# Optimization experiments

Hardware: AMD Instinct MI355X
Metric: run time of the kernel (lower is better)

## Reference

```python
import jax, jax.numpy as jnp
import numpy as np

C = 512  # in_channels

def _maxpool2x2(t):
    # t: [B, c, H, W] -> [B, c, H//2, W//2]
    B, c, H, W = t.shape
    return t.reshape(B, c, H // 2, 2, W // 2, 2).max(axis=(3, 5))

def setup_inputs() -> dict:
    key = jax.random.key(0)
    ks = jax.random.split(key, 6)
    B, H, W = 16, 64, 64
    x = jax.random.normal(ks[0], (B, C, H, W), dtype=jnp.float32)
    # 1x1 conv weights (spectral norm is just a static rescale of the weight;
    # we model the post-normalized weight directly). Shapes: [out_c, in_c].
    scale = 0.02
    w_theta = jax.random.normal(ks[1], (C // 8, C), dtype=jnp.float32) * scale
    w_phi = jax.random.normal(ks[2], (C // 8, C), dtype=jnp.float32) * scale
    w_g = jax.random.normal(ks[3], (C // 2, C), dtype=jnp.float32) * scale
    w_o = jax.random.normal(ks[4], (C, C // 2), dtype=jnp.float32) * scale
    gamma = jnp.asarray(0.5, dtype=jnp.float32)  # nonzero so attention path matters
    return {"x": x, "w_theta": w_theta, "w_phi": w_phi, "w_g": w_g,
            "w_o": w_o, "gamma": gamma}

def reference(x, w_theta, w_phi, w_g, w_o, gamma):
    B, c, H, W = x.shape
    N = H * W
    M = N // 4
    # 1x1 convs == channel matmuls
    theta = jnp.einsum('oc,bchw->bohw', w_theta, x)            # [B, C/8, H, W]
    phi = _maxpool2x2(jnp.einsum('oc,bchw->bohw', w_phi, x))   # [B, C/8, H/2, W/2]
    g = _maxpool2x2(jnp.einsum('oc,bchw->bohw', w_g, x))       # [B, C/2, H/2, W/2]
    theta = theta.reshape(B, c // 8, N)
    phi = phi.reshape(B, c // 8, M)
    g = g.reshape(B, c // 2, M)
    # attention: softmax over keys (last dim)
    scores = jnp.einsum('bdn,bdm->bnm', theta, phi)            # [B, N, M]
    beta = jax.nn.softmax(scores, axis=-1)
    o = jnp.einsum('bvm,bnm->bvn', g, beta)                    # [B, C/2, N]
    o = o.reshape(B, c // 2, H, W)
    o = jnp.einsum('ov,bvhw->bohw', w_o, o)                    # [B, C, H, W]
    return gamma * o + x
```

## Files before the change

kernel.cpp:

```cpp
#include <hip/hip_runtime.h>
#include <hip/hip_fp16.h>

typedef unsigned int u32;
typedef unsigned short u16;
typedef u32 __attribute__((may_alias)) u32a;
typedef u16 __attribute__((may_alias)) u16a;
typedef uint4 __attribute__((may_alias)) uint4a;
typedef uint2 __attribute__((may_alias)) uint2a;
typedef float __attribute__((may_alias)) f32a;
typedef float4 __attribute__((may_alias)) float4a;

typedef __attribute__((ext_vector_type(8))) short short8v;
typedef __attribute__((ext_vector_type(4))) float float4v;

union Frag { uint4 q; short8v s; u16 u[8]; };
union F4 { float4 v; float f[4]; };

#define BATCH 16
#define CIN   512
#define NPIX  4096
#define DD    64
#define VV    256
#define MM    1024

__device__ __forceinline__ float b2f(u16 u) {
  union { u32 i; float f; } v; v.i = ((u32)u) << 16; return v.f;
}
__device__ __forceinline__ u16 f2b(float f) {
  union { float f; u32 i; } v; v.f = f;
  u32 u = v.i;
  u32 r = (u + 0x7fffu + ((u >> 16) & 1u)) >> 16;
  return (u16)r;
}
__device__ __forceinline__ u16 f2h(float f) { return __half_as_ushort(__float2half(f)); }
__device__ __forceinline__ float h2f(u16 u) { return __half2float(__ushort_as_half(u)); }

__device__ __forceinline__ u32 cvtpk(float lo, float hi) {
  u32 r;
  asm("v_cvt_pk_bf16_f32 %0, %1, %2" : "=v"(r) : "v"(lo), "v"(hi));
  return r;
}

__device__ __forceinline__ float dot2(u32 a, u32 b, float c) {
  union { u32 i; float f; } a0, a1, b0, b1;
  a0.i = a << 16; a1.i = a & 0xffff0000u;
  b0.i = b << 16; b1.i = b & 0xffff0000u;
  return fmaf(a1.f, b1.f, fmaf(a0.f, b0.f, c));
}

__global__ __launch_bounds__(256) void k_detect(const void* __restrict__ x,
                                                u32* __restrict__ meta) {
  __shared__ int bad[256];
  const int t = threadIdx.x;
  float f = b2f(((const u16a*)x)[2 * t]);
  float a = fabsf(f);
  bad[t] = (a >= 1e-6f && a <= 100.f) ? 0 : 1;
  __syncthreads();
  if (t == 0) {
    int s = 0;
#pragma unroll 16
    for (int i = 0; i < 256; ++i) s += bad[i];
    meta[0] = (s > 64) ? 1u : 0u;
  }
}

__global__ __launch_bounds__(256) void k_cvt(
    const void* __restrict__ wt, const void* __restrict__ wp,
    const void* __restrict__ wg, const void* __restrict__ wo,
    const void* __restrict__ gm, const u32* __restrict__ meta,
    u16* __restrict__ wbf, float* __restrict__ gout) {
  const int flag = (int)meta[0];
  const int i = blockIdx.x * 256 + threadIdx.x;
  const void* src; int j;
  if (i < 32768)       { src = wt; j = i; }
  else if (i < 65536)  { src = wp; j = i - 32768; }
  else if (i < 196608) { src = wg; j = i - 65536; }
  else                 { src = wo; j = i - 196608; }
  wbf[i] = flag ? f2b(((const f32a*)src)[j]) : ((const u16a*)src)[j];
  if (i == 0)
    gout[0] = flag ? ((const f32a*)gm)[0] : b2f(((const u16a*)gm)[0]);
}

__global__ __launch_bounds__(256) void k_proj(
    const void* __restrict__ x, const u16* __restrict__ w_all,
    const u32* __restrict__ meta,
    u16* __restrict__ theta, u16* __restrict__ phi_t, u16* __restrict__ g)
{
  __shared__ __align__(16) u16 xs[128][136];
  const int tid  = threadIdx.x;
  const int lane = tid & 63;
  const int wv   = tid >> 6;
  const int lg   = lane >> 4;
  const int lr   = lane & 15;
  const int blk  = blockIdx.x;
  const int b    = blk >> 5;
  const int pxt  = blk & 31;
  const int n0   = pxt * 128;
  const int rbase = wv * 96;
  const int flag = (int)meta[0];

  float4v acc[6][8];
#pragma unroll
  for (int i = 0; i < 6; ++i)
#pragma unroll
    for (int j = 0; j < 8; ++j) acc[i][j] = (float4v){0.f, 0.f, 0.f, 0.f};

  const int pg = tid & 15;
  const int cg = tid >> 4;

  for (int cc = 0; cc < 4; ++cc) {
    const int c0 = cc * 128;
    __syncthreads();
    if (flag) {
      const f32a* src = (const f32a*)x +
          ((size_t)(b * CIN + c0 + cg * 8)) * NPIX + n0 + pg * 4;
#pragma unroll
      for (int cq = 0; cq < 2; ++cq) {
        const f32a* s4 = src + (size_t)(cq * 4) * NPIX;
        F4 a0, a1, a2, a3, b0, b1, b2, b3;
        a0.v = *(const float4a*)(s4);
        b0.v = *(const float4a*)(s4 + 64);
        a1.v = *(const float4a*)(s4 + NPIX);
        b1.v = *(const float4a*)(s4 + NPIX + 64);
        a2.v = *(const float4a*)(s4 + 2 * (size_t)NPIX);
        b2.v = *(const float4a*)(s4 + 2 * (size_t)NPIX + 64);
        a3.v = *(const float4a*)(s4 + 3 * (size_t)NPIX);
        b3.v = *(const float4a*)(s4 + 3 * (size_t)NPIX + 64);
        const int colb = cg * 8 + cq * 4;
#pragma unroll
        for (int j = 0; j < 4; ++j) {
          uint2 wd; wd.x = cvtpk(a0.f[j], a1.f[j]); wd.y = cvtpk(a2.f[j], a3.f[j]);
          *(uint2a*)&xs[pg * 4 + j][colb] = wd;
          uint2 vd; vd.x = cvtpk(b0.f[j], b1.f[j]); vd.y = cvtpk(b2.f[j], b3.f[j]);
          *(uint2a*)&xs[64 + pg * 4 + j][colb] = vd;
        }
      }
    } else {
#pragma unroll 8
      for (int it = 0; it < 64; ++it) {
        int idx = tid + it * 256;
        int cl = idx >> 7, px = idx & 127;
        xs[px][cl] = ((const u16a*)x)[((size_t)(b * CIN + c0 + cl)) * NPIX + (n0 + px)];
      }
    }
    __syncthreads();

#pragma unroll
    for (int kk = 0; kk < 4; ++kk) {
      short8v bfr[8];
#pragma unroll
      for (int pt = 0; pt < 8; ++pt) {
        Frag f; f.q = *(const uint4a*)&xs[pt * 16 + lr][kk * 32 + lg * 8];
        bfr[pt] = f.s;
      }
#pragma unroll
      for (int rt = 0; rt < 6; ++rt) {
        Frag af;
        af.q = *(const uint4a*)(w_all +
            (size_t)(rbase + rt * 16 + lr) * CIN + c0 + kk * 32 + lg * 8);
#pragma unroll
        for (int pt = 0; pt < 8; ++pt)
          acc[rt][pt] = __builtin_amdgcn_mfma_f32_16x16x32_bf16(af.s, bfr[pt], acc[rt][pt], 0, 0, 0);
      }
    }
  }

#pragma unroll
  for (int rt = 0; rt < 6; ++rt) {
    const int rowb = rbase + rt * 16;
    if (rowb < 64) {
#pragma unroll
      for (int pt = 0; pt < 8; ++pt)
#pragma unroll
        for (int r = 0; r < 4; ++r) {
          int row = rowb + lg * 4 + r;
          theta[((size_t)(b * DD + row)) * NPIX + n0 + pt * 16 + lr] = f2b(acc[rt][pt][r]);
        }
    } else {
#pragma unroll
      for (int pt = 0; pt < 4; ++pt)
#pragma unroll
        for (int r = 0; r < 4; ++r) {
          int row = rowb + lg * 4 + r;
          float pm = fmaxf(acc[rt][pt][r], acc[rt][pt + 4][r]);
          float po = fmaxf(pm, __shfl_xor(pm, 1));
          if (!(lr & 1)) {
            int m = pxt * 32 + pt * 8 + (lr >> 1);
            if (row < 128) phi_t[((size_t)(b * MM + m)) * DD + (row - 64)] = f2b(po);
            else           g[((size_t)(b * VV + (row - 128))) * MM + m]    = f2b(po);
          }
        }
    }
  }
}

__global__ __launch_bounds__(512, 4) void k_attn2(
    const u16* __restrict__ theta, const u16* __restrict__ phi_t,
    const u16* __restrict__ g, u16* __restrict__ o_t)
{
  __shared__ __align__(16) u32 sc[32 * 516];
  __shared__ float pmax8[32][8];
  __shared__ float psum[32][16];
  __shared__ float sinv_s[32];

  const int tid  = threadIdx.x;
  const int lane = tid & 63;
  const int wv   = tid >> 6;
  const int lg   = lane >> 4;
  const int lr   = lane & 15;
  const int bid  = blockIdx.x;
  const int swz  = ((bid & 7) << 8) | (bid >> 3);
  const int b    = swz >> 7;
  const int bqt  = swz & 127;
  const int nq0  = bqt * 32;

  u16a* sc16 = (u16a*)sc;

  short8v qa[2][2];
#pragma unroll
  for (int qt = 0; qt < 2; ++qt)
#pragma unroll
    for (int kk = 0; kk < 2; ++kk) {
      Frag f;
#pragma unroll
      for (int i = 0; i < 8; ++i) {
        int d = kk * 32 + lg * 8 + i;
        f.u[i] = theta[((size_t)(b * DD + d)) * NPIX + nq0 + qt * 16 + lr];
      }
      qa[qt][kk] = f.s;
    }

  {
    float mx0 = -3.0e38f, mx1 = -3.0e38f;
    const u16* ptw = phi_t + ((size_t)(b * MM) + wv * 128 + lr) * DD + lg * 8;
    uint4 f0 = *(const uint4a*)(ptw);
    uint4 f1 = *(const uint4a*)(ptw + 32);
#pragma unroll
    for (int mt = 0; mt < 8; ++mt) {
      const int mtn = (mt < 7) ? mt + 1 : 7;
      uint4 n0v = *(const uint4a*)(ptw + (size_t)mtn * 16 * DD);
      uint4 n1v = *(const uint4a*)(ptw + (size_t)mtn * 16 * DD + 32);
      Frag a0; a0.q = f0; Frag a1; a1.q = f1;
      float4v s0 = {0.f, 0.f, 0.f, 0.f}, s1 = {0.f, 0.f, 0.f, 0.f};
      s0 = __builtin_amdgcn_mfma_f32_16x16x32_bf16(a0.s, qa[0][0], s0, 0, 0, 0);
      s0 = __builtin_amdgcn_mfma_f32_16x16x32_bf16(a1.s, qa[0][1], s0, 0, 0, 0);
      s1 = __builtin_amdgcn_mfma_f32_16x16x32_bf16(a0.s, qa[1][0], s1, 0, 0, 0);
      s1 = __builtin_amdgcn_mfma_f32_16x16x32_bf16(a1.s, qa[1][1], s1, 0, 0, 0);
      float c0 = fminf(fmaxf(s0[0], -6.0e4f), 6.0e4f);
      float c1 = fminf(fmaxf(s0[1], -6.0e4f), 6.0e4f);
      float c2 = fminf(fmaxf(s0[2], -6.0e4f), 6.0e4f);
      float c3 = fminf(fmaxf(s0[3], -6.0e4f), 6.0e4f);
      mx0 = fmaxf(mx0, fmaxf(fmaxf(c0, c1), fmaxf(c2, c3)));
      uint2 w0;
      w0.x = (u32)f2h(c0) | ((u32)f2h(c1) << 16);
      w0.y = (u32)f2h(c2) | ((u32)f2h(c3) << 16);
      *(uint2a*)&sc16[(size_t)lr * 1032 + wv * 128 + mt * 16 + lg * 4] = w0;
      float d0 = fminf(fmaxf(s1[0], -6.0e4f), 6.0e4f);
      float d1 = fminf(fmaxf(s1[1], -6.0e4f), 6.0e4f);
      float d2 = fminf(fmaxf(s1[2], -6.0e4f), 6.0e4f);
      float d3 = fminf(fmaxf(s1[3], -6.0e4f), 6.0e4f);
      mx1 = fmaxf(mx1, fmaxf(fmaxf(d0, d1), fmaxf(d2, d3)));
      uint2 w1;
      w1.x = (u32)f2h(d0) | ((u32)f2h(d1) << 16);
      w1.y = (u32)f2h(d2) | ((u32)f2h(d3) << 16);
      *(uint2a*)&sc16[(size_t)(16 + lr) * 1032 + wv * 128 + mt * 16 + lg * 4] = w1;
      f0 = n0v; f1 = n1v;
    }
    mx0 = fmaxf(mx0, __shfl_xor(mx0, 16));
    mx0 = fmaxf(mx0, __shfl_xor(mx0, 32));
    mx1 = fmaxf(mx1, __shfl_xor(mx1, 16));
    mx1 = fmaxf(mx1, __shfl_xor(mx1, 32));
    if (lane < 16) {
      pmax8[lr][wv]      = mx0;
      pmax8[16 + lr][wv] = mx1;
    }
  }
  __syncthreads();

  const int q  = tid & 31;
  const int sg = tid >> 5;
  {
    float maxq = pmax8[q][0];
#pragma unroll
    for (int i = 1; i < 8; ++i) maxq = fmaxf(maxq, pmax8[q][i]);
    float ssum = 0.f;
#pragma unroll 4
    for (int kp = 0; kp < 32; ++kp) {
      int kk = (kp + sg) & 31;
      int idx = q * 516 + sg * 32 + kk;
      u32 raw = sc[idx];
      float f0 = h2f((u16)(raw & 0xffffu));
      float f1 = h2f((u16)(raw >> 16));
      float e0 = __expf(fminf(f0 - maxq, 0.f));
      float e1 = __expf(fminf(f1 - maxq, 0.f));
      ssum += e0 + e1;
      sc[idx] = (u32)f2b(e0) | ((u32)f2b(e1) << 16);
    }
    psum[q][sg] = ssum;
    __syncthreads();
    float tot = 0.f;
#pragma unroll
    for (int i = 0; i < 16; ++i) tot += psum[q][i];
    if (sg == 0) sinv_s[q] = 1.f / tot;
  }
  __syncthreads();

  {
    const u16* gv0 = g + (size_t)b * (VV * MM) + ((size_t)(wv * 32) + lr) * MM + lg * 8;
    const u16* gv1 = gv0 + (size_t)16 * MM;
    const u16* p0b = sc16 + (size_t)lr * 1032 + lg * 8;
    const u16* p1b = p0b + (size_t)16 * 1032;

    float4v a00 = {0.f,0.f,0.f,0.f}, a01 = {0.f,0.f,0.f,0.f};
    float4v a10 = {0.f,0.f,0.f,0.f}, a11 = {0.f,0.f,0.f,0.f};

    uint4 ga0 = *(const uint4a*)(gv0);
    uint4 ga1 = *(const uint4a*)(gv1);
    uint4 pa0 = *(const uint4a*)(p0b);
    uint4 pa1 = *(const uint4a*)(p1b);
    uint4 gb0 = *(const uint4a*)(gv0 + 32);
    uint4 gb1 = *(const uint4a*)(gv1 + 32);
    uint4 pb0 = *(const uint4a*)(p0b + 32);
    uint4 pb1 = *(const uint4a*)(p1b + 32);

#pragma unroll 4
    for (int ms = 0; ms < 32; ms += 2) {
      const int m2 = (ms + 2 < 32) ? ms + 2 : 30;
      const int m3 = (ms + 3 < 32) ? ms + 3 : 31;
      uint4 gc0 = *(const uint4a*)(gv0 + m2 * 32);
      uint4 gc1 = *(const uint4a*)(gv1 + m2 * 32);
      uint4 pc0 = *(const uint4a*)(p0b + m2 * 32);
      uint4 pc1 = *(const uint4a*)(p1b + m2 * 32);
      {
        Frag x0, x1, y0, y1; x0.q = ga0; x1.q = ga1; y0.q = pa0; y1.q = pa1;
        a00 = __builtin_amdgcn_mfma_f32_16x16x32_bf16(x0.s, y0.s, a00, 0, 0, 0);
        a01 = __builtin_amdgcn_mfma_f32_16x16x32_bf16(x0.s, y1.s, a01, 0, 0, 0);
        a10 = __builtin_amdgcn_mfma_f32_16x16x32_bf16(x1.s, y0.s, a10, 0, 0, 0);
        a11 = __builtin_amdgcn_mfma_f32_16x16x32_bf16(x1.s, y1.s, a11, 0, 0, 0);
      }
      uint4 gd0 = *(const uint4a*)(gv0 + m3 * 32);
      uint4 gd1 = *(const uint4a*)(gv1 + m3 * 32);
      uint4 pd0 = *(const uint4a*)(p0b + m3 * 32);
      uint4 pd1 = *(const uint4a*)(p1b + m3 * 32);
      {
        Frag x0, x1, y0, y1; x0.q = gb0; x1.q = gb1; y0.q = pb0; y1.q = pb1;
        a00 = __builtin_amdgcn_mfma_f32_16x16x32_bf16(x0.s, y0.s, a00, 0, 0, 0);
        a01 = __builtin_amdgcn_mfma_f32_16x16x32_bf16(x0.s, y1.s, a01, 0, 0, 0);
        a10 = __builtin_amdgcn_mfma_f32_16x16x32_bf16(x1.s, y0.s, a10, 0, 0, 0);
        a11 = __builtin_amdgcn_mfma_f32_16x16x32_bf16(x1.s, y1.s, a11, 0, 0, 0);
      }
      ga0 = gc0; ga1 = gc1; pa0 = pc0; pa1 = pc1;
      gb0 = gd0; gb1 = gd1; pb0 = pd0; pb1 = pd1;
    }

    const float si0 = sinv_s[lr];
    const float si1 = sinv_s[16 + lr];
    {
      uint2 wd;
      wd.x = cvtpk(a00[0] * si0, a00[1] * si0);
      wd.y = cvtpk(a00[2] * si0, a00[3] * si0);
      *(uint2a*)(o_t + ((size_t)(b * NPIX + nq0 + lr)) * VV + wv * 32 + lg * 4) = wd;
      wd.x = cvtpk(a01[0] * si1, a01[1] * si1);
      wd.y = cvtpk(a01[2] * si1, a01[3] * si1);
      *(uint2a*)(o_t + ((size_t)(b * NPIX + nq0 + 16 + lr)) * VV + wv * 32 + lg * 4) = wd;
      wd.x = cvtpk(a10[0] * si0, a10[1] * si0);
      wd.y = cvtpk(a10[2] * si0, a10[3] * si0);
      *(uint2a*)(o_t + ((size_t)(b * NPIX + nq0 + lr)) * VV + wv * 32 + 16 + lg * 4) = wd;
      wd.x = cvtpk(a11[0] * si1, a11[1] * si1);
      wd.y = cvtpk(a11[2] * si1, a11[3] * si1);
      *(uint2a*)(o_t + ((size_t)(b * NPIX + nq0 + 16 + lr)) * VV + wv * 32 + 16 + lg * 4) = wd;
    }
  }
}

__global__ __launch_bounds__(256, 4) void k_oproj(
    const u16* __restrict__ o_t, const u16* __restrict__ wo,
    const void* __restrict__ x, const float* __restrict__ gamma_p,
    const u32* __restrict__ meta, void* __restrict__ out)
{
  const int tid  = threadIdx.x;
  const int lane = tid & 63;
  const int wv   = tid >> 6;
  const int lg   = lane >> 4;
  const int lr   = lane & 15;
  const int bid  = blockIdx.x;
  const int swz  = ((bid & 7) << 9) | (bid >> 3);
  const int b    = swz >> 8;
  const int nt   = (swz >> 1) & 127;
  const int och  = swz & 1;
  const int n0   = nt * 32;
  const int ocb  = och * 256 + wv * 64;
  const int flag = (int)meta[0];

  float4v acc[4][2];
#pragma unroll
  for (int j = 0; j < 4; ++j)
#pragma unroll
    for (int t = 0; t < 2; ++t) acc[j][t] = (float4v){0.f, 0.f, 0.f, 0.f};

  const u16* obl = o_t + ((size_t)(b * NPIX) + n0 + lr) * VV;
  const u16* wbl = wo + (size_t)(ocb + lr) * VV;

#pragma unroll 2
  for (int kk = 0; kk < 8; ++kk) {
    const int ko = kk * 32 + lg * 8;
    Frag a0, a1, w0, w1, w2, w3;
    a0.q = *(const uint4a*)(obl + ko);
    a1.q = *(const uint4a*)(obl + (size_t)16 * VV + ko);
    w0.q = *(const uint4a*)(wbl + ko);
    w1.q = *(const uint4a*)(wbl + (size_t)16 * VV + ko);
    w2.q = *(const uint4a*)(wbl + (size_t)32 * VV + ko);
    w3.q = *(const uint4a*)(wbl + (size_t)48 * VV + ko);
    acc[0][0] = __builtin_amdgcn_mfma_f32_16x16x32_bf16(a0.s, w0.s, acc[0][0], 0, 0, 0);
    acc[0][1] = __builtin_amdgcn_mfma_f32_16x16x32_bf16(a1.s, w0.s, acc[0][1], 0, 0, 0);
    acc[1][0] = __builtin_amdgcn_mfma_f32_16x16x32_bf16(a0.s, w1.s, acc[1][0], 0, 0, 0);
    acc[1][1] = __builtin_amdgcn_mfma_f32_16x16x32_bf16(a1.s, w1.s, acc[1][1], 0, 0, 0);
    acc[2][0] = __builtin_amdgcn_mfma_f32_16x16x32_bf16(a0.s, w2.s, acc[2][0], 0, 0, 0);
    acc[2][1] = __builtin_amdgcn_mfma_f32_16x16x32_bf16(a1.s, w2.s, acc[2][1], 0, 0, 0);
    acc[3][0] = __builtin_amdgcn_mfma_f32_16x16x32_bf16(a0.s, w3.s, acc[3][0], 0, 0, 0);
    acc[3][1] = __builtin_amdgcn_mfma_f32_16x16x32_bf16(a1.s, w3.s, acc[3][1], 0, 0, 0);
  }

  const float gmv = gamma_p[0];
#pragma unroll
  for (int j = 0; j < 4; ++j) {
    const int oc = ocb + j * 16 + lr;
#pragma unroll
    for (int t = 0; t < 2; ++t) {
      const size_t off = ((size_t)(b * CIN + oc)) * NPIX + n0 + t * 16 + lg * 4;
      if (flag) {
        F4 xv; xv.v = *(const float4a*)((const f32a*)x + off);
        F4 o;
        o.f[0] = gmv * acc[j][t][0] + xv.f[0];
        o.f[1] = gmv * acc[j][t][1] + xv.f[1];
        o.f[2] = gmv * acc[j][t][2] + xv.f[2];
        o.f[3] = gmv * acc[j][t][3] + xv.f[3];
        *(float4a*)((f32a*)out + off) = o.v;
      } else {
        uint2 xv = *(const uint2a*)((const u16a*)x + off);
        uint2 st;
        st.x = (u32)f2b(gmv * acc[j][t][0] + b2f((u16)(xv.x & 0xffffu))) |
               ((u32)f2b(gmv * acc[j][t][1] + b2f((u16)(xv.x >> 16))) << 16);
        st.y = (u32)f2b(gmv * acc[j][t][2] + b2f((u16)(xv.y & 0xffffu))) |
               ((u32)f2b(gmv * acc[j][t][3] + b2f((u16)(xv.y >> 16))) << 16);
        *(uint2a*)((u16a*)out + off) = st;
      }
    }
  }
}

__global__ __launch_bounds__(256) void k_attn(
    const u16* __restrict__ theta, const u16* __restrict__ phi_t,
    const u16* __restrict__ g, const u16* __restrict__ wo,
    const void* __restrict__ x, const float* __restrict__ gamma_p,
    const u32* __restrict__ meta, void* __restrict__ out)
{
  __shared__ __align__(16) u32 sc[16 * 516];
  __shared__ __align__(16) u16 ot[16 * 264];
  __shared__ float pmax[16][16];
  __shared__ float psum[16][16];
  __shared__ float sinv_s[16];

  const int tid  = threadIdx.x;
  const int lane = tid & 63;
  const int wv   = tid >> 6;
  const int lg   = lane >> 4;
  const int lr   = lane & 15;
  const int blk  = blockIdx.x;
  const int b    = blk >> 8;
  const int qt   = blk & 255;
  const int nq0  = qt * 16;
  const int flag = (int)meta[0];

  u16a* sc16 = (u16a*)sc;

  short8v qa[2];
#pragma unroll
  for (int kk = 0; kk < 2; ++kk) {
    Frag f;
#pragma unroll
    for (int i = 0; i < 8; ++i) {
      int d = kk * 32 + lg * 8 + i;
      f.u[i] = theta[((size_t)(b * DD + d)) * NPIX + nq0 + lr];
    }
    qa[kk] = f.s;
  }

  {
    const u16* pt = phi_t + (size_t)b * (MM * DD);
#pragma unroll 2
    for (int mt = 0; mt < 16; ++mt) {
      const int m0 = wv * 256 + mt * 16;
      float4v s = {0.f, 0.f, 0.f, 0.f};
#pragma unroll
      for (int kk = 0; kk < 2; ++kk) {
        Frag f; f.q = *(const uint4a*)(pt + (size_t)(m0 + lr) * DD + kk * 32 + lg * 8);
        s = __builtin_amdgcn_mfma_f32_16x16x32_bf16(qa[kk], f.s, s, 0, 0, 0);
      }
#pragma unroll
      for (int r = 0; r < 4; ++r) {
        int qq = lg * 4 + r;
        float v = fminf(fmaxf(s[r], -6.0e4f), 6.0e4f);
        sc16[qq * 1032 + m0 + lr] = f2h(v);
      }
    }
  }
  __syncthreads();

  {
    const int q  = tid & 15;
    const int sg = tid >> 4;
    float mx = -3.0e38f;
#pragma unroll 8
    for (int k = 0; k < 64; ++k) {
      int kk = (k + sg * 2) & 63;
      mx = fmaxf(mx, h2f(sc16[q * 1032 + sg * 64 + kk]));
    }
    pmax[q][sg] = mx;
    __syncthreads();
    float maxq = -3.0e38f;
#pragma unroll
    for (int i = 0; i < 16; ++i) maxq = fmaxf(maxq, pmax[q][i]);
    float ssum = 0.f;
#pragma unroll 4
    for (int kp = 0; kp < 32; ++kp) {
      int kk = (kp + sg) & 31;
      int idx = q * 516 + sg * 32 + kk;
      u32 raw = sc[idx];
      float f0 = h2f((u16)(raw & 0xffffu));
      float f1 = h2f((u16)(raw >> 16));
      float e0 = __expf(fminf(f0 - maxq, 0.f));
      float e1 = __expf(fminf(f1 - maxq, 0.f));
      ssum += e0 + e1;
      sc[idx] = (u32)f2b(e0) | ((u32)f2b(e1) << 16);
    }
    psum[q][sg] = ssum;
    __syncthreads();
    float tot = 0.f;
#pragma unroll
    for (int i = 0; i < 16; ++i) tot += psum[q][i];
    if (sg == 0) sinv_s[q] = 1.f / tot;
  }
  __syncthreads();

  const int q  = tid & 15;
  const int sg = tid >> 4;
  {
    float4v oacc[4];
#pragma unroll
    for (int i = 0; i < 4; ++i) oacc[i] = (float4v){0.f, 0.f, 0.f, 0.f};
    const u16* gb = g + (size_t)b * (VV * MM);
#pragma unroll 2
    for (int ms = 0; ms < 32; ++ms) {
      Frag pf; pf.q = *(const uint4a*)(sc16 + lr * 1032 + ms * 32 + lg * 8);
#pragma unroll
      for (int vt = 0; vt < 4; ++vt) {
        Frag gf; gf.q = *(const uint4a*)(gb + (size_t)(wv * 64 + vt * 16 + lr) * MM + ms * 32 + lg * 8);
        oacc[vt] = __builtin_amdgcn_mfma_f32_16x16x32_bf16(gf.s, pf.s, oacc[vt], 0, 0, 0);
      }
    }
    const float si = sinv_s[lr];
#pragma unroll
    for (int vt = 0; vt < 4; ++vt) {
      u32 lo = (u32)f2b(oacc[vt][0] * si) | ((u32)f2b(oacc[vt][1] * si) << 16);
      u32 hi = (u32)f2b(oacc[vt][2] * si) | ((u32)f2b(oacc[vt][3] * si) << 16);
      u32a* p = (u32a*)&ot[lr * 264 + wv * 64 + vt * 16 + lg * 4];
      p[0] = lo; p[1] = hi;
    }
  }
  __syncthreads();

  {
    short8v ob[8];
#pragma unroll
    for (int ks = 0; ks < 8; ++ks) {
      Frag f; f.q = *(const uint4a*)(ot + lr * 264 + ks * 32 + lg * 8);
      ob[ks] = f.s;
    }
    const float gmv = gamma_p[0];
    const int oc0 = wv * 128;
#pragma unroll 2
    for (int oct = 0; oct < 8; ++oct) {
      float4v c = {0.f, 0.f, 0.f, 0.f};
#pragma unroll
      for (int ks = 0; ks < 8; ++ks) {
        Frag f; f.q = *(const uint4a*)(wo + (size_t)(oc0 + oct * 16 + lr) * VV + ks * 32 + lg * 8);
        c = __builtin_amdgcn_mfma_f32_16x16x32_bf16(f.s, ob[ks], c, 0, 0, 0);
      }
#pragma unroll
      for (int r = 0; r < 4; ++r) {
        int oc = oc0 + oct * 16 + lg * 4 + r;
        size_t off = ((size_t)(b * CIN + oc)) * NPIX + nq0 + lr;
        if (flag) {
          ((f32a*)out)[off] = gmv * c[r] + ((const f32a*)x)[off];
        } else {
          ((u16a*)out)[off] = f2b(gmv * c[r] + b2f(((const u16a*)x)[off]));
        }
      }
    }
  }
}

extern "C" void kernel_launch(void* const* d_in, const int* in_sizes, int n_in,
                              void* d_out, int out_size, void* d_ws, size_t ws_size,
                              hipStream_t stream) {
  (void)in_sizes; (void)n_in; (void)out_size;
  const void* x  = d_in[0];
  const void* wt = d_in[1];
  const void* wp = d_in[2];
  const void* wg = d_in[3];
  const void* wo = d_in[4];
  const void* gm = d_in[5];

  u16* theta = (u16*)d_ws;
  u16* phi_t = theta + (size_t)BATCH * DD * NPIX;
  u16* g     = phi_t + (size_t)BATCH * MM * DD;
  u16* wbf   = g     + (size_t)BATCH * VV * MM;
  float* gamma_f = (float*)(wbf + 327680);
  u32* meta      = (u32*)(gamma_f + 1);
  u16* o_t   = (u16*)d_ws + 9764896;
  const size_t need = ((size_t)9764896 + (size_t)BATCH * NPIX * VV) * 2;

  hipLaunchKernelGGL(k_detect, dim3(1), dim3(256), 0, stream, x, meta);
  hipLaunchKernelGGL(k_cvt, dim3(1280), dim3(256), 0, stream,
                     wt, wp, wg, wo, gm, meta, wbf, gamma_f);
  hipLaunchKernelGGL(k_proj, dim3(BATCH * 32), dim3(256), 0, stream,
                     x, wbf, meta, theta, phi_t, g);
  if (ws_size >= need) {
    hipLaunchKernelGGL(k_attn2, dim3(BATCH * 128), dim3(512), 0, stream,
                       theta, phi_t, g, o_t);
    hipLaunchKernelGGL(k_oproj, dim3(BATCH * 256), dim3(256), 0, stream,
                       o_t, wbf + 196608, x, gamma_f, meta, d_out);
  } else {
    hipLaunchKernelGGL(k_attn, dim3(BATCH * 256), dim3(256), 0, stream,
                       theta, phi_t, g, wbf + 196608, x, gamma_f, meta, d_out);
  }
}
```

Measured before the change: 570.2 us.

## Keep attention scores in registers and fuse softmax exp into per-wave epilogue

Raw QK scores now stay in registers across the max-reduction barrier instead of being stored to LDS as fp16 and re-read. Each wave then computes the exponentials for its own tile, writes bf16 probabilities into an XOR-swizzled LDS buffer, and reduces the row sums per wave. This drops one LDS round trip, one barrier, and the fp16 clamp/convert path. It also adds s_setprio around the PV MFMA groups. The cost is 64 extra VGPRs per thread for the held scores, which may hurt occupancy under the 512x4 launch bound.

```diff
diff --git a/kernel.cpp b/kernel.cpp
--- a/kernel.cpp
+++ b/kernel.cpp
@@ -198,10 +198,9 @@
     const u16* __restrict__ theta, const u16* __restrict__ phi_t,
     const u16* __restrict__ g, u16* __restrict__ o_t)
 {
-  __shared__ __align__(16) u32 sc[32 * 516];
+  __shared__ __align__(16) u16 sc16[32 * 1024];
   __shared__ float pmax8[32][8];
-  __shared__ float psum[32][16];
-  __shared__ float sinv_s[32];
+  __shared__ float psum[32][8];
 
   const int tid  = threadIdx.x;
   const int lane = tid & 63;
@@ -213,8 +212,7 @@
   const int b    = swz >> 7;
   const int bqt  = swz & 127;
   const int nq0  = bqt * 32;
-
-  u16a* sc16 = (u16a*)sc;
+  const int swzm = (lr & 7) << 3;
 
   short8v qa[2][2];
 #pragma unroll
@@ -230,6 +228,7 @@
       qa[qt][kk] = f.s;
     }
 
+  float4v sS0[8], sS1[8];
   {
     float mx0 = -3.0e38f, mx1 = -3.0e38f;
     const u16* ptw = phi_t + ((size_t)(b * MM) + wv * 128 + lr) * DD + lg * 8;
@@ -246,24 +245,9 @@
       s0 = __builtin_amdgcn_mfma_f32_16x16x32_bf16(a1.s, qa[0][1], s0, 0, 0, 0);
       s1 = __builtin_amdgcn_mfma_f32_16x16x32_bf16(a0.s, qa[1][0], s1, 0, 0, 0);
       s1 = __builtin_amdgcn_mfma_f32_16x16x32_bf16(a1.s, qa[1][1], s1, 0, 0, 0);
-      float c0 = fminf(fmaxf(s0[0], -6.0e4f), 6.0e4f);
-      float c1 = fminf(fmaxf(s0[1], -6.0e4f), 6.0e4f);
-      float c2 = fminf(fmaxf(s0[2], -6.0e4f), 6.0e4f);
-      float c3 = fminf(fmaxf(s0[3], -6.0e4f), 6.0e4f);
-      mx0 = fmaxf(mx0, fmaxf(fmaxf(c0, c1), fmaxf(c2, c3)));
-      uint2 w0;
-      w0.x = (u32)f2h(c0) | ((u32)f2h(c1) << 16);
-      w0.y = (u32)f2h(c2) | ((u32)f2h(c3) << 16);
-      *(uint2a*)&sc16[(size_t)lr * 1032 + wv * 128 + mt * 16 + lg * 4] = w0;
-      float d0 = fminf(fmaxf(s1[0], -6.0e4f), 6.0e4f);
-      float d1 = fminf(fmaxf(s1[1], -6.0e4f), 6.0e4f);
-      float d2 = fminf(fmaxf(s1[2], -6.0e4f), 6.0e4f);
-      float d3 = fminf(fmaxf(s1[3], -6.0e4f), 6.0e4f);
-      mx1 = fmaxf(mx1, fmaxf(fmaxf(d0, d1), fmaxf(d2, d3)));
-      uint2 w1;
-      w1.x = (u32)f2h(d0) | ((u32)f2h(d1) << 16);
-      w1.y = (u32)f2h(d2) | ((u32)f2h(d3) << 16);
-      *(uint2a*)&sc16[(size_t)(16 + lr) * 1032 + wv * 128 + mt * 16 + lg * 4] = w1;
+      sS0[mt] = s0; sS1[mt] = s1;
+      mx0 = fmaxf(mx0, fmaxf(fmaxf(s0[0], s0[1]), fmaxf(s0[2], s0[3])));
+      mx1 = fmaxf(mx1, fmaxf(fmaxf(s1[0], s1[1]), fmaxf(s1[2], s1[3])));
       f0 = n0v; f1 = n1v;
     }
     mx0 = fmaxf(mx0, __shfl_xor(mx0, 16));
@@ -277,51 +261,60 @@
   }
   __syncthreads();
 
-  const int q  = tid & 31;
-  const int sg = tid >> 5;
   {
-    float maxq = pmax8[q][0];
-#pragma unroll
-    for (int i = 1; i < 8; ++i) maxq = fmaxf(maxq, pmax8[q][i]);
-    float ssum = 0.f;
-#pragma unroll 4
-    for (int kp = 0; kp < 32; ++kp) {
-      int kk = (kp + sg) & 31;
-      int idx = q * 516 + sg * 32 + kk;
-      u32 raw = sc[idx];
-      float f0 = h2f((u16)(raw & 0xffffu));
-      float f1 = h2f((u16)(raw >> 16));
-      float e0 = __expf(fminf(f0 - maxq, 0.f));
-      float e1 = __expf(fminf(f1 - maxq, 0.f));
-      ssum += e0 + e1;
-      sc[idx] = (u32)f2b(e0) | ((u32)f2b(e1) << 16);
-    }
-    psum[q][sg] = ssum;
-    __syncthreads();
-    float tot = 0.f;
-#pragma unroll
-    for (int i = 0; i < 16; ++i) tot += psum[q][i];
-    if (sg == 0) sinv_s[q] = 1.f / tot;
+    float maxq0 = pmax8[lr][0];
+    float maxq1 = pmax8[16 + lr][0];
+#pragma unroll
+    for (int i = 1; i < 8; ++i) {
+      maxq0 = fmaxf(maxq0, pmax8[lr][i]);
+      maxq1 = fmaxf(maxq1, pmax8[16 + lr][i]);
+    }
+    float sum0 = 0.f, sum1 = 0.f;
+#pragma unroll
+    for (int mt = 0; mt < 8; ++mt) {
+      const int mbase = wv * 128 + mt * 16 + lg * 4;
+      const int midx  = mbase ^ swzm;
+      float e0 = __expf(sS0[mt][0] - maxq0);
+      float e1 = __expf(sS0[mt][1] - maxq0);
+      float e2 = __expf(sS0[mt][2] - maxq0);
+      float e3 = __expf(sS0[mt][3] - maxq0);
+      sum0 += (e0 + e1) + (e2 + e3);
+      uint2 w0; w0.x = cvtpk(e0, e1); w0.y = cvtpk(e2, e3);
+      *(uint2a*)&sc16[(size_t)lr * 1024 + midx] = w0;
+      float d0 = __expf(sS1[mt][0] - maxq1);
+      float d1 = __expf(sS1[mt][1] - maxq1);
+      float d2 = __expf(sS1[mt][2] - maxq1);
+      float d3 = __expf(sS1[mt][3] - maxq1);
+      sum1 += (d0 + d1) + (d2 + d3);
+      uint2 w1; w1.x = cvtpk(d0, d1); w1.y = cvtpk(d2, d3);
+      *(uint2a*)&sc16[(size_t)(16 + lr) * 1024 + midx] = w1;
+    }
+    sum0 += __shfl_xor(sum0, 16); sum0 += __shfl_xor(sum0, 32);
+    sum1 += __shfl_xor(sum1, 16); sum1 += __shfl_xor(sum1, 32);
+    if (lane < 16) {
+      psum[lr][wv]      = sum0;
+      psum[16 + lr][wv] = sum1;
+    }
   }
   __syncthreads();
 
   {
     const u16* gv0 = g + (size_t)b * (VV * MM) + ((size_t)(wv * 32) + lr) * MM + lg * 8;
     const u16* gv1 = gv0 + (size_t)16 * MM;
-    const u16* p0b = sc16 + (size_t)lr * 1032 + lg * 8;
-    const u16* p1b = p0b + (size_t)16 * 1032;
+    const u16* p0b = sc16 + (size_t)lr * 1024;
+    const u16* p1b = sc16 + (size_t)(16 + lr) * 1024;
 
     float4v a00 = {0.f,0.f,0.f,0.f}, a01 = {0.f,0.f,0.f,0.f};
     float4v a10 = {0.f,0.f,0.f,0.f}, a11 = {0.f,0.f,0.f,0.f};
 
     uint4 ga0 = *(const uint4a*)(gv0);
     uint4 ga1 = *(const uint4a*)(gv1);
-    uint4 pa0 = *(const uint4a*)(p0b);
-    uint4 pa1 = *(const uint4a*)(p1b);
+    uint4 pa0 = *(const uint4a*)(p0b + ((lg * 8) ^ swzm));
+    uint4 pa1 = *(const uint4a*)(p1b + ((lg * 8) ^ swzm));
     uint4 gb0 = *(const uint4a*)(gv0 + 32);
     uint4 gb1 = *(const uint4a*)(gv1 + 32);
-    uint4 pb0 = *(const uint4a*)(p0b + 32);
-    uint4 pb1 = *(const uint4a*)(p1b + 32);
+    uint4 pb0 = *(const uint4a*)(p0b + ((32 + lg * 8) ^ swzm));
+    uint4 pb1 = *(const uint4a*)(p1b + ((32 + lg * 8) ^ swzm));
 
 #pragma unroll 4
     for (int ms = 0; ms < 32; ms += 2) {
@@ -329,32 +322,39 @@
       const int m3 = (ms + 3 < 32) ? ms + 3 : 31;
       uint4 gc0 = *(const uint4a*)(gv0 + m2 * 32);
       uint4 gc1 = *(const uint4a*)(gv1 + m2 * 32);
-      uint4 pc0 = *(const uint4a*)(p0b + m2 * 32);
-      uint4 pc1 = *(const uint4a*)(p1b + m2 * 32);
+      uint4 pc0 = *(const uint4a*)(p0b + ((m2 * 32 + lg * 8) ^ swzm));
+      uint4 pc1 = *(const uint4a*)(p1b + ((m2 * 32 + lg * 8) ^ swzm));
       {
         Frag x0, x1, y0, y1; x0.q = ga0; x1.q = ga1; y0.q = pa0; y1.q = pa1;
+        __builtin_amdgcn_s_setprio(1);
         a00 = __builtin_amdgcn_mfma_f32_16x16x32_bf16(x0.s, y0.s, a00, 0, 0, 0);
         a01 = __builtin_amdgcn_mfma_f32_16x16x32_bf16(x0.s, y1.s, a01, 0, 0, 0);
         a10 = __builtin_amdgcn_mfma_f32_16x16x32_bf16(x1.s, y0.s, a10, 0, 0, 0);
         a11 = __builtin_amdgcn_mfma_f32_16x16x32_bf16(x1.s, y1.s, a11, 0, 0, 0);
+        __builtin_amdgcn_s_setprio(0);
       }
       uint4 gd0 = *(const uint4a*)(gv0 + m3 * 32);
       uint4 gd1 = *(const uint4a*)(gv1 + m3 * 32);
-      uint4 pd0 = *(const uint4a*)(p0b + m3 * 32);
-      uint4 pd1 = *(const uint4a*)(p1b + m3 * 32);
+      uint4 pd0 = *(const uint4a*)(p0b + ((m3 * 32 + lg * 8) ^ swzm));
+      uint4 pd1 = *(const uint4a*)(p1b + ((m3 * 32 + lg * 8) ^ swzm));
       {
         Frag x0, x1, y0, y1; x0.q = gb0; x1.q = gb1; y0.q = pb0; y1.q = pb1;
+        __builtin_amdgcn_s_setprio(1);
         a00 = __builtin_amdgcn_mfma_f32_16x16x32_bf16(x0.s, y0.s, a00, 0, 0, 0);
         a01 = __builtin_amdgcn_mfma_f32_16x16x32_bf16(x0.s, y1.s, a01, 0, 0, 0);
         a10 = __builtin_amdgcn_mfma_f32_16x16x32_bf16(x1.s, y0.s, a10, 0, 0, 0);
         a11 = __builtin_amdgcn_mfma_f32_16x16x32_bf16(x1.s, y1.s, a11, 0, 0, 0);
+        __builtin_amdgcn_s_setprio(0);
       }
       ga0 = gc0; ga1 = gc1; pa0 = pc0; pa1 = pc1;
       gb0 = gd0; gb1 = gd1; pb0 = pd0; pb1 = pd1;
     }
 
-    const float si0 = sinv_s[lr];
-    const float si1 = sinv_s[16 + lr];
+    float t0 = 0.f, t1 = 0.f;
+#pragma unroll
+    for (int i = 0; i < 8; ++i) { t0 += psum[lr][i]; t1 += psum[16 + lr][i]; }
+    const float si0 = 1.f / t0;
+    const float si1 = 1.f / t1;
     {
       uint2 wd;
       wd.x = cvtpk(a00[0] * si0, a00[1] * si0);
```

Result: no change. 577.0 us (+1.2%).
